# Kernel optimization log

Hardware: AMD Instinct MI355X
Metric: run time of the kernel (lower is better)

Reference implementation:

```python
import jax, jax.numpy as jnp
import numpy as np

QBITS = 8
QP = float(2 ** (QBITS - 1) - 1)  # 127 for 8-bit symmetric quantization


def quant(x, K):
    # learned-scale symmetric uniform quantization (fake-quant / dequant),
    # straight-through estimator for gradients
    xc = jnp.clip(x / K, -1.0, 1.0)
    q = jnp.round(xc * QP) / QP
    return (xc + jax.lax.stop_gradient(q - xc)) * K


def setup_inputs() -> dict:
    key = jax.random.key(0)
    k0, k1, k2 = jax.random.split(key, 3)
    B, S, D, H = 64, 197, 768, 3072  # ViT-B/16: 197 tokens, d=768, mlp=3072
    hidden_state = jax.random.normal(k0, (B, S, D), jnp.float32)
    # xavier-uniform-like scale for weights
    W1 = jax.random.normal(k1, (H, D), jnp.float32) * np.float32(1.0 / np.sqrt(D))
    b1 = jnp.zeros((H,), jnp.float32)
    W2 = jax.random.normal(k2, (D, H), jnp.float32) * np.float32(1.0 / np.sqrt(H))
    b2 = jnp.zeros((D,), jnp.float32)
    # learned per-layer activation / weight scale factors (kmlp_* lists)
    ka1 = jnp.array([3.0], jnp.float32)
    kw1 = jnp.array([0.1], jnp.float32)
    ka2 = jnp.array([3.0], jnp.float32)
    kw2 = jnp.array([0.1], jnp.float32)
    return {"hidden_state": hidden_state, "W1": W1, "b1": b1, "W2": W2,
            "b2": b2, "ka1": ka1, "kw1": kw1, "ka2": ka2, "kw2": kw2}


def reference(hidden_state, W1, b1, W2, b2, ka1, kw1, ka2, kw2):
    # fc1: quantize activations with Ka, weights with Kw, then GEMM + bias
    h = jnp.einsum("bsd,hd->bsh", quant(hidden_state, ka1), quant(W1, kw1)) + b1
    h = jax.nn.gelu(h, approximate=False)  # F.gelu default = exact erf
    # dropout is identity in eval mode
    out = jnp.einsum("bsh,dh->bsd", quant(h, ka2), quant(W2, kw2)) + b2
    return out
```

## Files before the change

kernel.cpp:

```cpp
#include <hip/hip_runtime.h>
#include <stdint.h>


typedef __attribute__((ext_vector_type(4))) int i32x4;

static constexpr int MROWS = 12608;
static constexpr int MPAD  = 12672;
static constexpr int DDIM  = 768;
static constexpr int HDIM  = 3072;

__device__ __forceinline__ int quant_one(float x, float K) {
    float xc = x / K;
    xc = fminf(fmaxf(xc, -1.0f), 1.0f);
    return (int)rintf(xc * 127.0f);
}

__global__ void quant_kernel(const float* __restrict__ x, int8_t* __restrict__ q,
                             const float* __restrict__ kp, int nvalid4, int ntot4) {
    int i = blockIdx.x * 256 + threadIdx.x;
    if (i >= ntot4) return;
    int packed = 0;
    if (i < nvalid4) {
        float K = kp[0];
        float4 v = reinterpret_cast<const float4*>(x)[i];
        packed = (quant_one(v.x, K) & 255)
               | ((quant_one(v.y, K) & 255) << 8)
               | ((quant_one(v.z, K) & 255) << 16)
               | ((quant_one(v.w, K) & 255) << 24);
    }
    reinterpret_cast<int*>(q)[i] = packed;
}

__device__ __forceinline__ void load16_to_lds(const int8_t* g, int8_t* l) {
    __builtin_amdgcn_global_load_lds(
        (const __attribute__((address_space(1))) void*)g,
        (__attribute__((address_space(3))) void*)l, 16, 0, 0);
}

template<int KD, int ND, bool EPI1>
__global__ __launch_bounds__(256)
void gemm_i8_kernel(const int8_t* __restrict__ A, const int8_t* __restrict__ B,
                    int8_t* __restrict__ qout, float* __restrict__ fout,
                    const float* __restrict__ bias,
                    const float* __restrict__ kA, const float* __restrict__ kW,
                    const float* __restrict__ kQ) {
    __shared__ __align__(16) int8_t Asm[128 * 64];
    __shared__ __align__(16) int8_t Bsm[128 * 64];

    const int tid  = threadIdx.x;
    const int lane = tid & 63;
    const int wave = tid >> 6;
    const int wr   = wave >> 1;
    const int wc   = wave & 1;
    const int bm   = blockIdx.y * 128;
    const int bn   = blockIdx.x * 128;

    i32x4 acc[4][4] = {};

    const int srow = tid >> 2;
    const int scol = (tid & 3) << 4;
    const int8_t* gA = A + (size_t)(bm + srow) * KD + scol;
    const int8_t* gB = B + (size_t)(bn + srow) * KD + scol;

    const int fr = lane & 15;
    const int kc = (lane >> 4) << 4;
    const int aoff = (wr * 64 + fr) * 64 + kc;
    const int boff = (wc * 64 + fr) * 64 + kc;

    for (int kt = 0; kt < KD; kt += 64) {
        load16_to_lds(gA + kt,                  Asm + 16 * tid);
        load16_to_lds(gA + (size_t)64 * KD + kt, Asm + 4096 + 16 * tid);
        load16_to_lds(gB + kt,                  Bsm + 16 * tid);
        load16_to_lds(gB + (size_t)64 * KD + kt, Bsm + 4096 + 16 * tid);
        __syncthreads();

        i32x4 af[4], bf[4];
#pragma unroll
        for (int m = 0; m < 4; ++m)
            af[m] = *reinterpret_cast<const i32x4*>(Asm + aoff + m * 1024);
#pragma unroll
        for (int n = 0; n < 4; ++n)
            bf[n] = *reinterpret_cast<const i32x4*>(Bsm + boff + n * 1024);
#pragma unroll
        for (int m = 0; m < 4; ++m)
#pragma unroll
            for (int n = 0; n < 4; ++n)
                acc[m][n] = __builtin_amdgcn_mfma_i32_16x16x64_i8(af[m], bf[n], acc[m][n], 0, 0, 0);
        __syncthreads();
    }

    const float sAW = kA[0] * kW[0] * (1.0f / 16129.0f);
    float kq = 1.0f;
    if constexpr (EPI1) kq = kQ[0];

    const int row0 = bm + wr * 64 + ((lane >> 4) << 2);
    const int col0 = bn + wc * 64 + fr;
#pragma unroll
    for (int m = 0; m < 4; ++m) {
#pragma unroll
        for (int n = 0; n < 4; ++n) {
            const int col = col0 + n * 16;
            const float bv = bias[col];
#pragma unroll
            for (int j = 0; j < 4; ++j) {
                const int row = row0 + m * 16 + j;
                float h = (float)acc[m][n][j] * sAW + bv;
                if constexpr (EPI1) {
                    float g  = 0.5f * h * (1.0f + erff(h * 0.70710678118654752f));
                    float xc = fminf(fmaxf(g / kq, -1.0f), 1.0f);
                    qout[(size_t)row * ND + col] = (int8_t)(int)rintf(xc * 127.0f);
                } else {
                    if (row < MROWS)
                        fout[(size_t)row * ND + col] = h;
                }
            }
        }
    }
}

extern "C" void kernel_launch(void* const* d_in, const int* in_sizes, int n_in,
                              void* d_out, int out_size, void* d_ws, size_t ws_size,
                              hipStream_t stream) {
    const float* hidden = (const float*)d_in[0];
    const float* W1     = (const float*)d_in[1];
    const float* b1     = (const float*)d_in[2];
    const float* W2     = (const float*)d_in[3];
    const float* b2     = (const float*)d_in[4];
    const float* ka1    = (const float*)d_in[5];
    const float* kw1    = (const float*)d_in[6];
    const float* ka2    = (const float*)d_in[7];
    const float* kw2    = (const float*)d_in[8];
    float* out = (float*)d_out;

    int8_t* a8  = (int8_t*)d_ws;
    int8_t* w1q = a8  + (size_t)MPAD * DDIM;
    int8_t* w2q = w1q + (size_t)HDIM * DDIM;
    int8_t* h8  = w2q + (size_t)DDIM * HDIM;

    {
        int ntot4 = MPAD * DDIM / 4, nval4 = MROWS * DDIM / 4;
        quant_kernel<<<(ntot4 + 255) / 256, 256, 0, stream>>>(hidden, a8, ka1, nval4, ntot4);
    }
    {
        int n4 = HDIM * DDIM / 4;
        quant_kernel<<<(n4 + 255) / 256, 256, 0, stream>>>(W1, w1q, kw1, n4, n4);
        quant_kernel<<<(n4 + 255) / 256, 256, 0, stream>>>(W2, w2q, kw2, n4, n4);
    }

    gemm_i8_kernel<DDIM, HDIM, true>
        <<<dim3(HDIM / 128, MPAD / 128), 256, 0, stream>>>
        (a8, w1q, h8, nullptr, b1, ka1, kw1, ka2);

    gemm_i8_kernel<HDIM, DDIM, false>
        <<<dim3(DDIM / 128, MPAD / 128), 256, 0, stream>>>
        (h8, w2q, nullptr, out, b2, ka2, kw2, nullptr);
}
```

Baseline: 252.7 us.

## Double-buffer LDS with 128-wide K tiles, XOR swizzle, and MFMA priority

Reworks the int8 GEMM main loop to prefetch the next K tile into a second LDS buffer while computing on the current one, which cuts the barriers per iteration to one. The K tile doubles to 128 and the LDS layout uses an XOR swizzle to avoid bank conflicts on the fragment reads. It also raises wave priority around the MFMA block and sets launch bounds to two blocks per CU. LDS use grows to 64KB per block, which may limit occupancy.

Result: no change. 254.5 us (+0.7%).

```diff
diff --git a/kernel.cpp b/kernel.cpp
--- a/kernel.cpp
+++ b/kernel.cpp
@@ -38,14 +38,13 @@
 }
 
 template<int KD, int ND, bool EPI1>
-__global__ __launch_bounds__(256)
+__global__ __launch_bounds__(256, 2)
 void gemm_i8_kernel(const int8_t* __restrict__ A, const int8_t* __restrict__ B,
                     int8_t* __restrict__ qout, float* __restrict__ fout,
                     const float* __restrict__ bias,
                     const float* __restrict__ kA, const float* __restrict__ kW,
                     const float* __restrict__ kQ) {
-    __shared__ __align__(16) int8_t Asm[128 * 64];
-    __shared__ __align__(16) int8_t Bsm[128 * 64];
+    __shared__ __align__(16) int8_t lds[2][2][128 * 128];
 
     const int tid  = threadIdx.x;
     const int lane = tid & 63;
@@ -57,43 +56,75 @@
 
     i32x4 acc[4][4] = {};
 
-    const int srow = tid >> 2;
-    const int scol = (tid & 3) << 4;
-    const int8_t* gA = A + (size_t)(bm + srow) * KD + scol;
-    const int8_t* gB = B + (size_t)(bn + srow) * KD + scol;
+    const int srow = tid >> 3;
+    const int soff = ((tid & 7) ^ (srow & 7)) << 4;
+    const int8_t* gA = A + (size_t)(bm + srow) * KD + soff;
+    const int8_t* gB = B + (size_t)(bn + srow) * KD + soff;
+    const int ldst = tid * 16;
+
+#define STAGE(buf, ktb)                                                        \
+    do {                                                                       \
+        const int8_t* a_ = gA + (ktb);                                         \
+        const int8_t* b_ = gB + (ktb);                                         \
+        int8_t* la_ = &lds[buf][0][ldst];                                      \
+        int8_t* lb_ = &lds[buf][1][ldst];                                      \
+        load16_to_lds(a_,                    la_);                             \
+        load16_to_lds(a_ + (size_t)32 * KD,  la_ + 4096);                      \
+        load16_to_lds(a_ + (size_t)64 * KD,  la_ + 8192);                      \
+        load16_to_lds(a_ + (size_t)96 * KD,  la_ + 12288);                     \
+        load16_to_lds(b_,                    lb_);                             \
+        load16_to_lds(b_ + (size_t)32 * KD,  lb_ + 4096);                      \
+        load16_to_lds(b_ + (size_t)64 * KD,  lb_ + 8192);                      \
+        load16_to_lds(b_ + (size_t)96 * KD,  lb_ + 12288);                     \
+    } while (0)
 
     const int fr = lane & 15;
-    const int kc = (lane >> 4) << 4;
-    const int aoff = (wr * 64 + fr) * 64 + kc;
-    const int boff = (wc * 64 + fr) * 64 + kc;
+    const int q4 = lane >> 4;
+    const int c0 = ((q4 ^ (fr & 7)) << 4);
+    int aoff[4], boff[4];
+#pragma unroll
+    for (int m = 0; m < 4; ++m) aoff[m] = (wr * 64 + m * 16 + fr) * 128 + c0;
+#pragma unroll
+    for (int n = 0; n < 4; ++n) boff[n] = (wc * 64 + n * 16 + fr) * 128 + c0;
 
-    for (int kt = 0; kt < KD; kt += 64) {
-        load16_to_lds(gA + kt,                  Asm + 16 * tid);
-        load16_to_lds(gA + (size_t)64 * KD + kt, Asm + 4096 + 16 * tid);
-        load16_to_lds(gB + kt,                  Bsm + 16 * tid);
-        load16_to_lds(gB + (size_t)64 * KD + kt, Bsm + 4096 + 16 * tid);
-        __syncthreads();
+    constexpr int NT = KD / 128;
+    STAGE(0, 0);
+    __syncthreads();
 
-        i32x4 af[4], bf[4];
+    int cur = 0;
+    for (int t = 0; t < NT; ++t) {
+        if (t + 1 < NT) STAGE(cur ^ 1, (t + 1) * 128);
+
+        const int8_t* Ab = &lds[cur][0][0];
+        const int8_t* Bb = &lds[cur][1][0];
 #pragma unroll
-        for (int m = 0; m < 4; ++m)
-            af[m] = *reinterpret_cast<const i32x4*>(Asm + aoff + m * 1024);
+        for (int ks = 0; ks < 2; ++ks) {
+            const int kx = ks << 6;
+            i32x4 af[4], bf[4];
 #pragma unroll
-        for (int n = 0; n < 4; ++n)
-            bf[n] = *reinterpret_cast<const i32x4*>(Bsm + boff + n * 1024);
-#pragma unroll
-        for (int m = 0; m < 4; ++m)
+            for (int m = 0; m < 4; ++m)
+                af[m] = *reinterpret_cast<const i32x4*>(Ab + (aoff[m] ^ kx));
 #pragma unroll
             for (int n = 0; n < 4; ++n)
-                acc[m][n] = __builtin_amdgcn_mfma_i32_16x16x64_i8(af[m], bf[n], acc[m][n], 0, 0, 0);
+                bf[n] = *reinterpret_cast<const i32x4*>(Bb + (boff[n] ^ kx));
+            __builtin_amdgcn_s_setprio(1);
+#pragma unroll
+            for (int m = 0; m < 4; ++m)
+#pragma unroll
+                for (int n = 0; n < 4; ++n)
+                    acc[m][n] = __builtin_amdgcn_mfma_i32_16x16x64_i8(af[m], bf[n], acc[m][n], 0, 0, 0);
+            __builtin_amdgcn_s_setprio(0);
+        }
         __syncthreads();
+        cur ^= 1;
     }
+#undef STAGE
 
     const float sAW = kA[0] * kW[0] * (1.0f / 16129.0f);
     float kq = 1.0f;
     if constexpr (EPI1) kq = kQ[0];
 
-    const int row0 = bm + wr * 64 + ((lane >> 4) << 2);
+    const int row0 = bm + wr * 64 + (q4 << 2);
     const int col0 = bn + wc * 64 + fr;
 #pragma unroll
     for (int m = 0; m < 4; ++m) {
```
